# Optimization experiments

Measured on AMD Instinct MI355X. Metric: run time of the kernel, lower is better.

## Reference

```python
import jax, jax.numpy as jnp
import numpy as np

V, S, D, H, L, F = 32000, 1024, 1024, 16, 6, 4096
DH = D // H          # 64
HALF = DH // 2       # 32
EPS = 1e-5
ROPE_BASE = 10000.0


def setup_inputs() -> dict:
    key = jax.random.key(0)
    ks = jax.random.split(key, 16)
    std = 0.02
    inp = {
        "tokens": jax.random.randint(ks[0], (4, S), 0, V),
        "tok_emb": jax.random.normal(ks[1], (V, D), jnp.float32) * std,
        "ln1_s": jnp.ones((L, D), jnp.float32),
        "ln1_b": jnp.zeros((L, D), jnp.float32),
        "w_qkv": jax.random.normal(ks[2], (L, D, 3 * D), jnp.float32) * std,
        "w_proj": jax.random.normal(ks[3], (L, D, D), jnp.float32) * std,
        "ln2_s": jnp.ones((L, D), jnp.float32),
        "ln2_b": jnp.zeros((L, D), jnp.float32),
        "w_in": jax.random.normal(ks[4], (L, D, 2 * F), jnp.float32) * std,
        "w_out": jax.random.normal(ks[5], (L, F, D), jnp.float32) * std,
        "lnf_s": jnp.ones((D,), jnp.float32),
        "lnf_b": jnp.zeros((D,), jnp.float32),
        "w_score": jax.random.normal(ks[6], (D, 1), jnp.float32) * std,
        "w_cls": jax.random.normal(ks[7], (D, S), jnp.float32) * std,
    }
    return inp


def _layernorm(x, s, b):
    m = x.mean(-1, keepdims=True)
    v = ((x - m) ** 2).mean(-1, keepdims=True)
    return (x - m) * jax.lax.rsqrt(v + EPS) * s + b


def _rotate_half(x):
    x_even = x[..., ::2]
    x_odd = x[..., 1::2]
    return jnp.stack((-x_odd, x_even), axis=-1).reshape(x.shape)


def _rope_tables():
    inv_freq = 1.0 / (ROPE_BASE ** (jnp.arange(0, DH, 2, dtype=jnp.float32) / DH))
    pos = jnp.arange(S, dtype=jnp.float32)
    freqs = jnp.outer(pos, inv_freq)               # [S, DH/2]
    cos = jnp.repeat(jnp.cos(freqs), 2, axis=-1)   # [S, DH]
    sin = jnp.repeat(jnp.sin(freqs), 2, axis=-1)
    return cos, sin


def _forward(tokens, tok_emb, ln1_s, ln1_b, w_qkv, w_proj, ln2_s, ln2_b,
             w_in, w_out, lnf_s, lnf_b, w_score, w_cls):
    B = tokens.shape[0]
    cos, sin = _rope_tables()                      # [S, DH], broadcast over B,H
    lower = jnp.tril(jnp.ones((S, S), jnp.bool_))  # j <= i -> "down" subspace
    scale = HALF ** -0.5

    h = tok_emb[tokens]                            # [B, S, D]

    def block(h, p):
        l1s, l1b, Wqkv, Wp, l2s, l2b, Wi, Wo = p
        # --- dual-triangle attention ---
        qkv = _layernorm(h, l1s, l1b) @ Wqkv       # [B, S, 3D]
        q, k, v = jnp.split(qkv, 3, axis=-1)
        def heads(t):
            return t.reshape(B, S, H, DH).transpose(0, 2, 1, 3)  # [B,H,S,DH]
        q, k, v = heads(q), heads(k), heads(v)
        q = q * cos + _rotate_half(q) * sin
        k = k * cos + _rotate_half(k) * sin
        a_up = jnp.einsum('bhqd,bhkd->bhqk', q[..., :HALF], k[..., :HALF]) * scale
        a_dn = jnp.einsum('bhqd,bhkd->bhqk', q[..., HALF:], k[..., HALF:]) * scale
        logits = jnp.where(lower, a_dn, a_up)
        w = jax.nn.softmax(logits, axis=-1)
        o = jnp.einsum('bhqk,bhkd->bhqd', w, v)
        o = o.transpose(0, 2, 1, 3).reshape(B, S, D) @ Wp
        h = h + o
        # --- SwiGLU MLP ---
        g = _layernorm(h, l2s, l2b) @ Wi           # [B, S, 2F]
        a, b = jnp.split(g, 2, axis=-1)
        h = h + (jax.nn.silu(a) * b) @ Wo
        return h, None

    h, _ = jax.lax.scan(block, h, (ln1_s, ln1_b, w_qkv, w_proj, ln2_s, ln2_b, w_in, w_out))

    # pooling head: per-position scores -> softmax over positions -> weighted sum
    h = _layernorm(h, lnf_s, lnf_b)
    scores = h @ w_score                           # [B, S, 1]
    pw = jax.nn.softmax(scores, axis=1)
    pooled = jnp.sum(pw * h, axis=1)               # [B, D]
    return pooled @ w_cls                          # [B, S] logits over positions


def reference(tokens, tok_emb, ln1_s, ln1_b, w_qkv, w_proj, ln2_s, ln2_b,
              w_in, w_out, lnf_s, lnf_b, w_score, w_cls):
    return _forward(tokens, tok_emb, ln1_s, ln1_b, w_qkv, w_proj, ln2_s, ln2_b,
                    w_in, w_out, lnf_s, lnf_b, w_score, w_cls)
```

## Files before the change

kernel.cpp:

```cpp
#include <hip/hip_runtime.h>

#define Bsz 4
#define Ssz 1024
#define Dsz 1024
#define Hn  16
#define DHn 64
#define Ln  6
#define Fsz 4096
#define SCALE_ 0.1767766952966369f
#define LOG2E_ 1.4426950408889634f

typedef unsigned long long u64;
typedef __attribute__((ext_vector_type(8))) short bf16x8;
typedef __attribute__((ext_vector_type(4))) float f32x4;

__device__ __forceinline__ unsigned short f2bf(float f) {
  union { float f; unsigned int u; } v; v.f = f;
  unsigned int u = v.u + 0x7fffu + ((v.u >> 16) & 1u);
  return (unsigned short)(u >> 16);
}
__device__ __forceinline__ float bf2f(unsigned short h) {
  union { unsigned int u; float f; } v; v.u = ((unsigned int)h) << 16;
  return v.f;
}
__device__ __forceinline__ void gload_lds16(const void* g, void* lds) {
  __builtin_amdgcn_global_load_lds(
      (const __attribute__((address_space(1))) unsigned int*)g,
      (__attribute__((address_space(3))) unsigned int*)lds, 16, 0, 0);
}

__device__ __forceinline__ int swz_addr(int r, int lq) {
  int line = r >> 1;
  int u = ((r & 1) << 2) | lq;
  int s = u ^ (line & 7);
  return line * 128 + s * 16;
}

__global__ __launch_bounds__(256) void k_cossin(float* __restrict__ cosT, float* __restrict__ sinT) {
  int idx = blockIdx.x * 256 + threadIdx.x;
  if (idx >= Ssz * 32) return;
  int s = idx >> 5, i = idx & 31;
  float inv = powf(10000.f, -((float)(2 * i)) / 64.f);
  float f = (float)s * inv;
  cosT[idx] = cosf(f);
  sinT[idx] = sinf(f);
}

__global__ __launch_bounds__(256) void k_embed(const int* __restrict__ tokens,
                                               const float* __restrict__ emb,
                                               float* __restrict__ h) {
  int rs = blockIdx.x;
  int t = threadIdx.x;
  int tok = tokens[rs];
  *(float4*)&h[(u64)rs * Dsz + t * 4] = *(const float4*)&emb[(u64)tok * Dsz + t * 4];
}

template <int BF16OUT>
__global__ __launch_bounds__(256) void k_layernorm(const float* __restrict__ x,
                                                   const float* __restrict__ sc,
                                                   const float* __restrict__ bi,
                                                   void* outv) {
  int row = blockIdx.x, t = threadIdx.x;
  const float* xr = x + (u64)row * Dsz;
  float4 v = *(const float4*)&xr[t * 4];
  float sm = v.x + v.y + v.z + v.w;
  float sq = v.x * v.x + v.y * v.y + v.z * v.z + v.w * v.w;
#pragma unroll
  for (int m = 1; m < 64; m <<= 1) { sm += __shfl_xor(sm, m); sq += __shfl_xor(sq, m); }
  __shared__ float r1[4], r2[4];
  if ((t & 63) == 0) { r1[t >> 6] = sm; r2[t >> 6] = sq; }
  __syncthreads();
  sm = r1[0] + r1[1] + r1[2] + r1[3];
  sq = r2[0] + r2[1] + r2[2] + r2[3];
  float mean = sm * (1.f / Dsz);
  float inv = rsqrtf(sq * (1.f / Dsz) - mean * mean + 1e-5f);
  float4 s4 = *(const float4*)&sc[t * 4];
  float4 b4 = *(const float4*)&bi[t * 4];
  float y0 = (v.x - mean) * inv * s4.x + b4.x;
  float y1 = (v.y - mean) * inv * s4.y + b4.y;
  float y2 = (v.z - mean) * inv * s4.z + b4.z;
  float y3 = (v.w - mean) * inv * s4.w + b4.w;
  if (BF16OUT) {
    ushort4 o; o.x = f2bf(y0); o.y = f2bf(y1); o.z = f2bf(y2); o.w = f2bf(y3);
    *(ushort4*)((unsigned short*)outv + (u64)row * Dsz + t * 4) = o;
  } else {
    float4 o; o.x = y0; o.y = y1; o.z = y2; o.w = y3;
    *(float4*)((float*)outv + (u64)row * Dsz + t * 4) = o;
  }
}

__global__ __launch_bounds__(256) void k_redres_ln(const float* __restrict__ p0,
                                                   const float* __restrict__ p1,
                                                   float* __restrict__ h,
                                                   const float* __restrict__ sc,
                                                   const float* __restrict__ bi,
                                                   unsigned short* __restrict__ xo) {
  int row = blockIdx.x, t = threadIdx.x;
  u64 base = (u64)row * Dsz + t * 4;
  float4 a = *(float4*)&h[base];
  float4 b0 = *(const float4*)&p0[base];
  float4 c0 = *(const float4*)&p1[base];
  a.x += b0.x + c0.x; a.y += b0.y + c0.y; a.z += b0.z + c0.z; a.w += b0.w + c0.w;
  *(float4*)&h[base] = a;
  float sm = a.x + a.y + a.z + a.w;
  float sq = a.x * a.x + a.y * a.y + a.z * a.z + a.w * a.w;
#pragma unroll
  for (int m = 1; m < 64; m <<= 1) { sm += __shfl_xor(sm, m); sq += __shfl_xor(sq, m); }
  __shared__ float r1[4], r2[4];
  if ((t & 63) == 0) { r1[t >> 6] = sm; r2[t >> 6] = sq; }
  __syncthreads();
  sm = r1[0] + r1[1] + r1[2] + r1[3];
  sq = r2[0] + r2[1] + r2[2] + r2[3];
  float mean = sm * (1.f / Dsz);
  float inv = rsqrtf(sq * (1.f / Dsz) - mean * mean + 1e-5f);
  float4 s4 = *(const float4*)&sc[t * 4];
  float4 b4 = *(const float4*)&bi[t * 4];
  ushort4 o;
  o.x = f2bf((a.x - mean) * inv * s4.x + b4.x);
  o.y = f2bf((a.y - mean) * inv * s4.y + b4.y);
  o.z = f2bf((a.z - mean) * inv * s4.z + b4.z);
  o.w = f2bf((a.w - mean) * inv * s4.w + b4.w);
  *(ushort4*)&xo[base] = o;
}

__global__ __launch_bounds__(256) void k_redres(const float* __restrict__ p0,
                                                const float* __restrict__ p1,
                                                float* __restrict__ h) {
  u64 i = ((u64)blockIdx.x * 256 + threadIdx.x) * 4;
  float4 a = *(float4*)&h[i];
  float4 b = *(const float4*)&p0[i];
  float4 c = *(const float4*)&p1[i];
  a.x += b.x + c.x; a.y += b.y + c.y; a.z += b.z + c.z; a.w += b.w + c.w;
  *(float4*)&h[i] = a;
}

__global__ __launch_bounds__(256) void k_wt(const float* __restrict__ in,
                                            unsigned short* __restrict__ out, int K, int N) {
  in += (u64)blockIdx.z * K * N;
  out += (u64)blockIdx.z * K * N;
  __shared__ float tile[32][33];
  int nb = blockIdx.x * 32, kb = blockIdx.y * 32;
  int t = threadIdx.x;
  int r = t >> 3, c4 = (t & 7) * 4;
  float4 v = *(const float4*)&in[(u64)(kb + r) * N + nb + c4];
  tile[r][c4] = v.x; tile[r][c4 + 1] = v.y; tile[r][c4 + 2] = v.z; tile[r][c4 + 3] = v.w;
  __syncthreads();
  ushort4 o;
  o.x = f2bf(tile[c4][r]); o.y = f2bf(tile[c4 + 1][r]);
  o.z = f2bf(tile[c4 + 2][r]); o.w = f2bf(tile[c4 + 3][r]);
  *(ushort4*)&out[(u64)(nb + r) * K + kb + c4] = o;
}

__global__ __launch_bounds__(256) void k_wt_pair(const float* __restrict__ in,
                                                 unsigned short* __restrict__ out) {
  in += (u64)blockIdx.z * Dsz * 2 * Fsz;
  out += (u64)blockIdx.z * 2 * Fsz * Dsz;
  __shared__ float tile[32][33];
  int nb = blockIdx.x * 32, kb = blockIdx.y * 32;
  int t = threadIdx.x;
  int r = t >> 3, c4 = (t & 7) * 4;
  int s0 = nb >> 1;
  int srccol = (c4 < 16) ? (s0 + c4) : (Fsz + s0 + (c4 - 16));
  float4 v = *(const float4*)&in[(u64)(kb + r) * (2 * Fsz) + srccol];
  tile[r][c4] = v.x; tile[r][c4 + 1] = v.y; tile[r][c4 + 2] = v.z; tile[r][c4 + 3] = v.w;
  __syncthreads();
  int sc = (r >> 1) + (r & 1) * 16;
  ushort4 o;
  o.x = f2bf(tile[c4][sc]); o.y = f2bf(tile[c4 + 1][sc]);
  o.z = f2bf(tile[c4 + 2][sc]); o.w = f2bf(tile[c4 + 3][sc]);
  *(ushort4*)&out[(u64)(nb + r) * Dsz + kb + c4] = o;
}

template <int EPI>
__global__ __launch_bounds__(256, 3)
void k_ring(const unsigned short* __restrict__ A,
            const unsigned short* __restrict__ Bt,
            const float* resid, void* Cout,
            int M, int N, int K, int KH,
            unsigned short* qr, unsigned short* kr, unsigned short* vt,
            const float* cosT, const float* sinT) {
  __shared__ char lds[3][16384] __attribute__((aligned(16)));
  int t = threadIdx.x, w = t >> 6, l = t & 63;
  int wm = w >> 1, wn = w & 1;
  int lr = l & 15, lq = l >> 4;
  int bn = blockIdx.x, bm = blockIdx.y, kz = blockIdx.z;
  int NT = KH >> 5;
  int g0 = t, g1 = t + 256;
  int L0 = g0 >> 3, u0 = (g0 & 7) ^ (L0 & 7), row0 = 2 * L0 + (u0 >> 2), kc0 = (u0 & 3) * 8;
  int L1 = g1 >> 3, u1 = (g1 & 7) ^ (L1 & 7), row1 = 2 * L1 + (u1 >> 2), kc1 = (u1 & 3) * 8;
  const unsigned short* Az = A + (u64)kz * KH;
  const unsigned short* Bz = Bt + (u64)kz * KH;
  const char* Asrc0 = (const char*)(Az + (u64)(bm * 128 + row0) * K + kc0);
  const char* Asrc1 = (const char*)(Az + (u64)(bm * 128 + row1) * K + kc1);
  const char* Bsrc0 = (const char*)(Bz + (u64)(bn * 128 + row0) * K + kc0);
  const char* Bsrc1 = (const char*)(Bz + (u64)(bn * 128 + row1) * K + kc1);
  f32x4 acc[4][4];
#pragma unroll
  for (int i = 0; i < 4; ++i)
#pragma unroll
    for (int j = 0; j < 4; ++j) acc[i][j] = (f32x4){0.f, 0.f, 0.f, 0.f};
#define STG(slot, jj) { char* d_ = lds[slot]; \
    gload_lds16(Asrc0 + (u64)(jj) * 64, d_ + g0 * 16); \
    gload_lds16(Asrc1 + (u64)(jj) * 64, d_ + g1 * 16); \
    gload_lds16(Bsrc0 + (u64)(jj) * 64, d_ + 8192 + g0 * 16); \
    gload_lds16(Bsrc1 + (u64)(jj) * 64, d_ + 8192 + g1 * 16); }
  STG(0, 0); STG(1, 1);
  int cs = 0, ss = 2;
  for (int j = 0; j < NT; ++j) {
    if (j < NT - 1) asm volatile("s_waitcnt vmcnt(4)" ::: "memory");
    else            asm volatile("s_waitcnt vmcnt(0)" ::: "memory");
    __builtin_amdgcn_s_barrier();
    __builtin_amdgcn_sched_barrier(0);
    const char* Ab = lds[cs];
    const char* Bb = lds[cs] + 8192;
    if (j + 2 < NT) STG(ss, j + 2);
    bf16x8 afrag[4], bfrag[4];
#pragma unroll
    for (int ni = 0; ni < 4; ++ni)
      bfrag[ni] = *(const bf16x8*)(Bb + swz_addr(wn * 64 + ni * 16 + lr, lq));
#pragma unroll
    for (int mi = 0; mi < 4; ++mi)
      afrag[mi] = *(const bf16x8*)(Ab + swz_addr(wm * 64 + mi * 16 + lr, lq));
    __builtin_amdgcn_s_setprio(1);
#pragma unroll
    for (int mi = 0; mi < 4; ++mi)
#pragma unroll
      for (int ni = 0; ni < 4; ++ni)
        acc[mi][ni] = __builtin_amdgcn_mfma_f32_16x16x32_bf16(afrag[mi], bfrag[ni], acc[mi][ni], 0, 0, 0);
    __builtin_amdgcn_s_setprio(0);
    cs = (cs == 2) ? 0 : cs + 1;
    ss = (ss == 2) ? 0 : ss + 1;
  }
#undef STG
  u64 zoff = (u64)kz * M * N;
#pragma unroll
  for (int mi = 0; mi < 4; ++mi)
#pragma unroll
    for (int ni = 0; ni < 4; ++ni)
#pragma unroll
      for (int r = 0; r < 4; ++r) {
        int row = bm * 128 + wm * 64 + mi * 16 + lq * 4 + r;
        int col = bn * 128 + wn * 64 + ni * 16 + lr;
        float v = acc[mi][ni][r];
        if (EPI == 3) {
          float pv = __shfl_xor(v, 1);
          if ((lr & 1) == 0) {
            float res = v / (1.f + __expf(-v)) * pv;
            ((unsigned short*)Cout)[(u64)row * (N >> 1) + (col >> 1)] = f2bf(res);
          }
        } else if (EPI == 4) {
          float pv = __shfl_xor(v, 1);
          int b = row >> 10, s = row & 1023;
          int sec = col >> 10, c = col & 1023, hh = c >> 6, dh = c & 63;
          if (sec == 2) {
            vt[((u64)(b * Hn + hh) * DHn + dh) * Ssz + s] = f2bf(v);
          } else {
            int ci = s * 32 + (dh >> 1);
            float cs_ = cosT[ci], sn_ = sinT[ci];
            float out = (dh & 1) ? (v * cs_ + pv * sn_) : (v * cs_ - pv * sn_);
            u64 dst = ((u64)(b * Hn + hh) * Ssz + s) * DHn + dh;
            (sec == 0 ? qr : kr)[dst] = f2bf(out);
          }
        } else {
          u64 idx = (u64)row * N + col;
          if (EPI == 0) ((float*)Cout)[zoff + idx] = v;
          else if (EPI == 1) ((unsigned short*)Cout)[idx] = f2bf(v);
          else ((float*)Cout)[idx] = resid[idx] + v;
        }
      }
}

__global__ __launch_bounds__(256) void k_attn(const unsigned short* __restrict__ qr,
                                              const unsigned short* __restrict__ kr,
                                              const unsigned short* __restrict__ vt,
                                              unsigned short* __restrict__ outp) {
  __shared__ unsigned short Klds[2][2][64 * 32] __attribute__((aligned(16)));
  __shared__ unsigned short Vlds[2][2][64 * 32] __attribute__((aligned(16)));
  __shared__ unsigned short Plds[4][16 * 64] __attribute__((aligned(16)));
  int qt = blockIdx.x, hh = blockIdx.y, b = blockIdx.z;
  int t = threadIdx.x, w = t >> 6, l = t & 63;
  int lr = l & 15, lq = l >> 4;
  u64 bh = (u64)(b * Hn + hh);
  const unsigned short* Qp = qr + bh * (Ssz * DHn);
  const unsigned short* Kp = kr + bh * (Ssz * DHn);
  const unsigned short* Vp = vt + bh * ((u64)DHn * Ssz);
  int q0 = qt * 64 + w * 16;
  bf16x8 qlo = *(const bf16x8*)&Qp[(q0 + lr) * DHn + lq * 8];
  bf16x8 qhi = *(const bf16x8*)&Qp[(q0 + lr) * DHn + 32 + lq * 8];
  int srow = t >> 2;
  int scol8 = (t & 3) * 8;
#define STAGEKV(bufi, kbase)                                                         \
  do {                                                                               \
    gload_lds16(&Kp[((kbase) + srow) * 64 + scol8],      (char*)&Klds[bufi][0][0] + t * 16); \
    gload_lds16(&Kp[((kbase) + srow) * 64 + 32 + scol8], (char*)&Klds[bufi][1][0] + t * 16); \
    gload_lds16(&Vp[(u64)srow * Ssz + (kbase) + scol8],      (char*)&Vlds[bufi][0][0] + t * 16); \
    gload_lds16(&Vp[(u64)srow * Ssz + (kbase) + 32 + scol8], (char*)&Vlds[bufi][1][0] + t * 16); \
  } while (0)
  float m_col = -1e30f, lsum = 0.f;
  float m_row[4] = {-1e30f, -1e30f, -1e30f, -1e30f};
  f32x4 o[4];
#pragma unroll
  for (int r = 0; r < 4; ++r) o[r] = (f32x4){0.f, 0.f, 0.f, 0.f};
  char* Pw = (char*)&Plds[w][0];

  STAGEKV(0, 0);
  asm volatile("s_waitcnt vmcnt(0)" ::: "memory");
  __syncthreads();
  int buf = 0;
  const float lsc = SCALE_ * LOG2E_;
  for (int kb = 0; kb < Ssz; kb += 64) {
    if (kb + 64 < Ssz) STAGEKV(buf ^ 1, kb + 64);
    float p[4][4];
#pragma unroll
    for (int ct = 0; ct < 4; ++ct) {
      int kc = kb + ct * 16;
      f32x4 z = (f32x4){0.f, 0.f, 0.f, 0.f};
      if (kc < q0) {
        bf16x8 khi = *(const bf16x8*)&Klds[buf][1][(ct * 16 + lr) * 32 + lq * 8];
        f32x4 shi = __builtin_amdgcn_mfma_f32_16x16x32_bf16(khi, qhi, z, 0, 0, 0);
#pragma unroll
        for (int r = 0; r < 4; ++r) p[ct][r] = shi[r] * lsc;
      } else if (kc > q0) {
        bf16x8 klo = *(const bf16x8*)&Klds[buf][0][(ct * 16 + lr) * 32 + lq * 8];
        f32x4 slo = __builtin_amdgcn_mfma_f32_16x16x32_bf16(klo, qlo, z, 0, 0, 0);
#pragma unroll
        for (int r = 0; r < 4; ++r) p[ct][r] = slo[r] * lsc;
      } else {
        bf16x8 klo = *(const bf16x8*)&Klds[buf][0][(ct * 16 + lr) * 32 + lq * 8];
        bf16x8 khi = *(const bf16x8*)&Klds[buf][1][(ct * 16 + lr) * 32 + lq * 8];
        f32x4 slo = __builtin_amdgcn_mfma_f32_16x16x32_bf16(klo, qlo, z, 0, 0, 0);
        f32x4 shi = __builtin_amdgcn_mfma_f32_16x16x32_bf16(khi, qhi, z, 0, 0, 0);
        int kg0 = kc + lq * 4;
        int qg = q0 + lr;
#pragma unroll
        for (int r = 0; r < 4; ++r) p[ct][r] = (kg0 + r <= qg ? shi[r] : slo[r]) * lsc;
      }
    }
    float tm = p[0][0];
#pragma unroll
    for (int ct = 0; ct < 4; ++ct)
#pragma unroll
      for (int r = 0; r < 4; ++r) tm = fmaxf(tm, p[ct][r]);
    tm = fmaxf(tm, __shfl_xor(tm, 16));
    tm = fmaxf(tm, __shfl_xor(tm, 32));
    if (__any(tm > m_col)) {
      float m_new = fmaxf(m_col, tm);
      lsum *= exp2f(m_col - m_new);
      m_col = m_new;
#pragma unroll
      for (int r = 0; r < 4; ++r) {
        float mr = __shfl(m_col, lq * 4 + r);
        float scf = exp2f(m_row[r] - mr);
        m_row[r] = mr;
        o[0][r] *= scf; o[1][r] *= scf; o[2][r] *= scf; o[3][r] *= scf;
      }
    }
#pragma unroll
    for (int ct = 0; ct < 4; ++ct) {
      float e0 = exp2f(p[ct][0] - m_col);
      float e1 = exp2f(p[ct][1] - m_col);
      float e2 = exp2f(p[ct][2] - m_col);
      float e3 = exp2f(p[ct][3] - m_col);
      lsum += e0 + e1 + e2 + e3;
      ushort4 pk; pk.x = f2bf(e0); pk.y = f2bf(e1); pk.z = f2bf(e2); pk.w = f2bf(e3);
      int byte_ = (lr * 128 + ct * 32 + lq * 8) ^ ((lr & 7) << 4);
      *(ushort4*)(Pw + byte_) = pk;
    }
    asm volatile("s_waitcnt lgkmcnt(0)" ::: "memory");
    __builtin_amdgcn_sched_barrier(0);
#pragma unroll
    for (int ks = 0; ks < 2; ++ks) {
      int pb = (lr * 128 + ks * 64 + lq * 16) ^ ((lr & 7) << 4);
      bf16x8 pa = *(const bf16x8*)(Pw + pb);
#pragma unroll
      for (int nt = 0; nt < 4; ++nt) {
        bf16x8 vb = *(const bf16x8*)&Vlds[buf][ks][(nt * 16 + lr) * 32 + lq * 8];
        o[nt] = __builtin_amdgcn_mfma_f32_16x16x32_bf16(pa, vb, o[nt], 0, 0, 0);
      }
    }
    asm volatile("s_waitcnt vmcnt(0)" ::: "memory");
    __syncthreads();
    buf ^= 1;
  }
  lsum += __shfl_xor(lsum, 16);
  lsum += __shfl_xor(lsum, 32);
  u64 obase = ((u64)b * Ssz) * Dsz + (u64)hh * DHn;
#pragma unroll
  for (int r = 0; r < 4; ++r) {
    float ls = __shfl(lsum, lq * 4 + r);
    float inv = 1.f / ls;
    int qrow = q0 + lq * 4 + r;
#pragma unroll
    for (int nt = 0; nt < 4; ++nt)
      outp[obase + (u64)qrow * Dsz + nt * 16 + lr] = f2bf(o[nt][r] * inv);
  }
#undef STAGEKV
}

__global__ __launch_bounds__(256) void k_scores(const float* __restrict__ hf,
                                                const float* __restrict__ wsc,
                                                float* __restrict__ scores) {
  int row = blockIdx.x * 4 + (threadIdx.x >> 6);
  int l = threadIdx.x & 63;
  const float* xr = hf + (u64)row * Dsz;
  float acc = 0.f;
#pragma unroll
  for (int j = 0; j < 4; ++j) {
    float4 v = *(const float4*)&xr[(j * 64 + l) * 4];
    float4 ww = *(const float4*)&wsc[(j * 64 + l) * 4];
    acc += v.x * ww.x + v.y * ww.y + v.z * ww.z + v.w * ww.w;
  }
#pragma unroll
  for (int m = 1; m < 64; m <<= 1) acc += __shfl_xor(acc, m);
  if (l == 0) scores[row] = acc;
}

__global__ __launch_bounds__(256) void k_softmax_s(const float* __restrict__ sc,
                                                   float* __restrict__ pw) {
  int b = blockIdx.x, t = threadIdx.x;
  const float* sr = sc + b * Ssz;
  float4 v = *(const float4*)&sr[t * 4];
  float mx = fmaxf(fmaxf(v.x, v.y), fmaxf(v.z, v.w));
#pragma unroll
  for (int m = 1; m < 64; m <<= 1) mx = fmaxf(mx, __shfl_xor(mx, m));
  __shared__ float red[4];
  if ((t & 63) == 0) red[t >> 6] = mx;
  __syncthreads();
  mx = fmaxf(fmaxf(red[0], red[1]), fmaxf(red[2], red[3]));
  float e0 = __expf(v.x - mx), e1 = __expf(v.y - mx), e2 = __expf(v.z - mx), e3 = __expf(v.w - mx);
  float sm = e0 + e1 + e2 + e3;
#pragma unroll
  for (int m = 1; m < 64; m <<= 1) sm += __shfl_xor(sm, m);
  __shared__ float red2[4];
  if ((t & 63) == 0) red2[t >> 6] = sm;
  __syncthreads();
  sm = red2[0] + red2[1] + red2[2] + red2[3];
  float inv = 1.f / sm;
  float4 o; o.x = e0 * inv; o.y = e1 * inv; o.z = e2 * inv; o.w = e3 * inv;
  *(float4*)&pw[b * Ssz + t * 4] = o;
}

__global__ __launch_bounds__(256) void k_pool1(const float* __restrict__ hf,
                                               const float* __restrict__ pw,
                                               float* __restrict__ part) {
  int d = blockIdx.x * 256 + threadIdx.x;
  int b = blockIdx.y, scn = blockIdx.z;
  const float* pwb = pw + b * Ssz + scn * 64;
  const float* hb = hf + ((u64)(b * Ssz + scn * 64)) * Dsz + d;
  float acc = 0.f;
#pragma unroll 4
  for (int s = 0; s < 64; ++s) acc += pwb[s] * hb[(u64)s * Dsz];
  part[(u64)(b * 16 + scn) * Dsz + d] = acc;
}
__global__ __launch_bounds__(256) void k_pool2(const float* __restrict__ part,
                                               float* __restrict__ pooled) {
  int d = blockIdx.x * 256 + threadIdx.x;
  int b = blockIdx.y;
  float acc = 0.f;
#pragma unroll
  for (int i = 0; i < 16; ++i) acc += part[(u64)(b * 16 + i) * Dsz + d];
  pooled[b * Dsz + d] = acc;
}

__global__ __launch_bounds__(256) void k_cls1(const float* __restrict__ pooled,
                                              const float* __restrict__ wcls,
                                              float* __restrict__ part) {
  int n = blockIdx.x * 64 + (threadIdx.x & 63);
  int b = threadIdx.x >> 6;
  int kz = blockIdx.y;
  const float* pb = pooled + b * Dsz + kz * 128;
  const float* wb = wcls + (u64)(kz * 128) * Ssz + n;
  float acc = 0.f;
#pragma unroll 4
  for (int k = 0; k < 128; ++k) acc += pb[k] * wb[(u64)k * Ssz];
  part[(u64)(kz * 4 + b) * Ssz + n] = acc;
}
__global__ __launch_bounds__(256) void k_cls2(const float* __restrict__ part,
                                              float* __restrict__ outp) {
  int n = blockIdx.x * 64 + (threadIdx.x & 63);
  int b = threadIdx.x >> 6;
  float acc = 0.f;
#pragma unroll
  for (int kz = 0; kz < 8; ++kz) acc += part[(u64)(kz * 4 + b) * Ssz + n];
  outp[b * Ssz + n] = acc;
}

extern "C" void kernel_launch(void* const* d_in, const int* in_sizes, int n_in,
                              void* d_out, int out_size, void* d_ws, size_t ws_size,
                              hipStream_t stream) {
  (void)in_sizes; (void)n_in; (void)out_size; (void)ws_size;
  const int*   tokens  = (const int*)  d_in[0];
  const float* tok_emb = (const float*)d_in[1];
  const float* ln1_s   = (const float*)d_in[2];
  const float* ln1_b   = (const float*)d_in[3];
  const float* w_qkv   = (const float*)d_in[4];
  const float* w_proj  = (const float*)d_in[5];
  const float* ln2_s   = (const float*)d_in[6];
  const float* ln2_b   = (const float*)d_in[7];
  const float* w_in    = (const float*)d_in[8];
  const float* w_out   = (const float*)d_in[9];
  const float* lnf_s   = (const float*)d_in[10];
  const float* lnf_b   = (const float*)d_in[11];
  const float* w_score = (const float*)d_in[12];
  const float* w_cls   = (const float*)d_in[13];
  float* outp = (float*)d_out;
  char* ws = (char*)d_ws;

  unsigned short* q_r    = (unsigned short*)(ws + 25165824ull);
  unsigned short* k_r    = (unsigned short*)(ws + 33554432ull);
  unsigned short* v_t    = (unsigned short*)(ws + 41943040ull);
  unsigned short* a_out  = (unsigned short*)(ws + 50331648ull);
  float*          hf     = (float*)(ws + 0);
  unsigned short* x_ln   = (unsigned short*)(ws + 67108864ull);
  unsigned short* mbuf   = (unsigned short*)(ws + 75497472ull);
  float*          h      = (float*)(ws + 109051904ull);
  float* cosT    = (float*)(ws + 125829120ull);
  float* sinT    = (float*)(ws + 125960192ull);
  float* scoresb = (float*)(ws + 126091264ull);
  float* pwb     = (float*)(ws + 126107648ull);
  float* pooledb = (float*)(ws + 126124032ull);
  float* poolpart= (float*)(ws + 126140416ull);
  float* clspart = (float*)(ws + 126402560ull);
  unsigned short* wqkv_t = (unsigned short*)(ws + 134217728ull);
  unsigned short* wproj_t= (unsigned short*)(ws + 171966464ull);
  unsigned short* win_t  = (unsigned short*)(ws + 184549376ull);
  unsigned short* wout_t = (unsigned short*)(ws + 285212672ull);
  float* skpart  = (float*)(ws + 335544320ull);

  dim3 blk(256);
  k_cossin<<<dim3(128), blk, 0, stream>>>(cosT, sinT);
  k_embed<<<dim3(4096), blk, 0, stream>>>(tokens, tok_emb, h);
  k_wt<<<dim3(96, 32, 6), blk, 0, stream>>>(w_qkv, wqkv_t, Dsz, 3 * Dsz);
  k_wt<<<dim3(32, 32, 6), blk, 0, stream>>>(w_proj, wproj_t, Dsz, Dsz);
  k_wt_pair<<<dim3(256, 32, 6), blk, 0, stream>>>(w_in, win_t);
  k_wt<<<dim3(32, 128, 6), blk, 0, stream>>>(w_out, wout_t, Fsz, Dsz);

  k_layernorm<1><<<dim3(4096), blk, 0, stream>>>(h, ln1_s, ln1_b, (void*)x_ln);
  for (int l = 0; l < Ln; ++l) {
    unsigned short* wq = wqkv_t + (u64)l * 3145728ull;
    unsigned short* wp = wproj_t + (u64)l * 1048576ull;
    unsigned short* wi = win_t + (u64)l * 8388608ull;
    unsigned short* wo = wout_t + (u64)l * 4194304ull;
    k_ring<4><<<dim3(24, 32), blk, 0, stream>>>(x_ln, wq, nullptr, nullptr,
        4096, 3072, 1024, 1024, q_r, k_r, v_t, cosT, sinT);
    k_attn<<<dim3(16, 16, 4), blk, 0, stream>>>(q_r, k_r, v_t, a_out);
    k_ring<2><<<dim3(8, 32), blk, 0, stream>>>(a_out, wp, h, (void*)h,
        4096, 1024, 1024, 1024, nullptr, nullptr, nullptr, nullptr, nullptr);
    k_layernorm<1><<<dim3(4096), blk, 0, stream>>>(h, ln2_s + l * Dsz, ln2_b + l * Dsz, (void*)x_ln);
    k_ring<3><<<dim3(64, 32), blk, 0, stream>>>(x_ln, wi, nullptr, (void*)mbuf,
        4096, 8192, 1024, 1024, nullptr, nullptr, nullptr, nullptr, nullptr);
    k_ring<0><<<dim3(8, 32, 2), blk, 0, stream>>>(mbuf, wo, nullptr, (void*)skpart,
        4096, 1024, 4096, 2048, nullptr, nullptr, nullptr, nullptr, nullptr);
    if (l < Ln - 1)
      k_redres_ln<<<dim3(4096), blk, 0, stream>>>(skpart, skpart + 4194304ull, h,
          ln1_s + (l + 1) * Dsz, ln1_b + (l + 1) * Dsz, x_ln);
    else
      k_redres<<<dim3(4096), blk, 0, stream>>>(skpart, skpart + 4194304ull, h);
  }

  k_layernorm<0><<<dim3(4096), blk, 0, stream>>>(h, lnf_s, lnf_b, (void*)hf);
  k_scores<<<dim3(1024), blk, 0, stream>>>(hf, w_score, scoresb);
  k_softmax_s<<<dim3(4), blk, 0, stream>>>(scoresb, pwb);
  k_pool1<<<dim3(4, 4, 16), blk, 0, stream>>>(hf, pwb, poolpart);
  k_pool2<<<dim3(4, 4), blk, 0, stream>>>(poolpart, pooledb);
  k_cls1<<<dim3(16, 8), blk, 0, stream>>>(pooledb, w_cls, clspart);
  k_cls2<<<dim3(16), blk, 0, stream>>>(clspart, outp);
}
```

Measured before the change: 1.963 ms.

## Add 256x256-tile pipelined GEMM kernel for MLP up/down projections

Introduces a new 512-thread GEMM kernel with 256x256 output tiles, double-buffered LDS staging via direct global-to-LDS loads, and explicit vmcnt waits interleaved with MFMA phases. The SwiGLU up-projection and the down-projection now use it, and the down-projection split-K goes from 2 to 4 partitions, so the residual-reduce kernels sum four partials. Larger tiles are meant to raise data reuse and MFMA density in the dominant MLP GEMMs. In exchange they use heavy register and LDS budgets and launch fewer blocks, and the extra split-K partials add memory traffic in the reduction.

```diff
diff --git a/kernel.cpp b/kernel.cpp
--- a/kernel.cpp
+++ b/kernel.cpp
@@ -34,6 +34,10 @@
   int u = ((r & 1) << 2) | lq;
   int s = u ^ (line & 7);
   return line * 128 + s * 16;
+}
+
+__device__ __forceinline__ bf16x8 frag_read(const char* base, int row, int lq) {
+  return *(const bf16x8*)(base + row * 64 + ((lq ^ (row & 3)) * 16));
 }
 
 __global__ __launch_bounds__(256) void k_cossin(float* __restrict__ cosT, float* __restrict__ sinT) {
@@ -89,8 +93,8 @@
   }
 }
 
-__global__ __launch_bounds__(256) void k_redres_ln(const float* __restrict__ p0,
-                                                   const float* __restrict__ p1,
+#define PARTN 4194304ull
+__global__ __launch_bounds__(256) void k_redres_ln(const float* __restrict__ p,
                                                    float* __restrict__ h,
                                                    const float* __restrict__ sc,
                                                    const float* __restrict__ bi,
@@ -98,9 +102,11 @@
   int row = blockIdx.x, t = threadIdx.x;
   u64 base = (u64)row * Dsz + t * 4;
   float4 a = *(float4*)&h[base];
-  float4 b0 = *(const float4*)&p0[base];
-  float4 c0 = *(const float4*)&p1[base];
-  a.x += b0.x + c0.x; a.y += b0.y + c0.y; a.z += b0.z + c0.z; a.w += b0.w + c0.w;
+#pragma unroll
+  for (int z = 0; z < 4; ++z) {
+    float4 q = *(const float4*)&p[z * PARTN + base];
+    a.x += q.x; a.y += q.y; a.z += q.z; a.w += q.w;
+  }
   *(float4*)&h[base] = a;
   float sm = a.x + a.y + a.z + a.w;
   float sq = a.x * a.x + a.y * a.y + a.z * a.z + a.w * a.w;
@@ -123,14 +129,15 @@
   *(ushort4*)&xo[base] = o;
 }
 
-__global__ __launch_bounds__(256) void k_redres(const float* __restrict__ p0,
-                                                const float* __restrict__ p1,
+__global__ __launch_bounds__(256) void k_redres(const float* __restrict__ p,
                                                 float* __restrict__ h) {
   u64 i = ((u64)blockIdx.x * 256 + threadIdx.x) * 4;
   float4 a = *(float4*)&h[i];
-  float4 b = *(const float4*)&p0[i];
-  float4 c = *(const float4*)&p1[i];
-  a.x += b.x + c.x; a.y += b.y + c.y; a.z += b.z + c.z; a.w += b.w + c.w;
+#pragma unroll
+  for (int z = 0; z < 4; ++z) {
+    float4 q = *(const float4*)&p[z * PARTN + i];
+    a.x += q.x; a.y += q.y; a.z += q.z; a.w += q.w;
+  }
   *(float4*)&h[i] = a;
 }
 
@@ -232,7 +239,6 @@
     ss = (ss == 2) ? 0 : ss + 1;
   }
 #undef STG
-  u64 zoff = (u64)kz * M * N;
 #pragma unroll
   for (int mi = 0; mi < 4; ++mi)
 #pragma unroll
@@ -242,13 +248,7 @@
         int row = bm * 128 + wm * 64 + mi * 16 + lq * 4 + r;
         int col = bn * 128 + wn * 64 + ni * 16 + lr;
         float v = acc[mi][ni][r];
-        if (EPI == 3) {
-          float pv = __shfl_xor(v, 1);
-          if ((lr & 1) == 0) {
-            float res = v / (1.f + __expf(-v)) * pv;
-            ((unsigned short*)Cout)[(u64)row * (N >> 1) + (col >> 1)] = f2bf(res);
-          }
-        } else if (EPI == 4) {
+        if (EPI == 4) {
           float pv = __shfl_xor(v, 1);
           int b = row >> 10, s = row & 1023;
           int sec = col >> 10, c = col & 1023, hh = c >> 6, dh = c & 63;
@@ -263,9 +263,124 @@
           }
         } else {
           u64 idx = (u64)row * N + col;
-          if (EPI == 0) ((float*)Cout)[zoff + idx] = v;
-          else if (EPI == 1) ((unsigned short*)Cout)[idx] = f2bf(v);
+          if (EPI == 1) ((unsigned short*)Cout)[idx] = f2bf(v);
           else ((float*)Cout)[idx] = resid[idx] + v;
+        }
+      }
+}
+
+#define VM8 asm volatile("s_waitcnt vmcnt(8)" ::: "memory")
+#define VM4 asm volatile("s_waitcnt vmcnt(4)" ::: "memory")
+#define VM0 asm volatile("s_waitcnt vmcnt(0)" ::: "memory")
+#define VMN
+
+#define STGP(buf_, kh_, j_) { \
+    char* dA = lds[buf_] + (kh_) * 16384; \
+    char* dB = lds[buf_] + 32768 + (kh_) * 16384; \
+    u64 ko = (u64)((j_) * 64 + (kh_) * 32) * 2; \
+    gload_lds16(Ab0 + ko, dA + t * 16); \
+    gload_lds16(Ab1 + ko, dA + 8192 + t * 16); \
+    gload_lds16(Bb0 + ko, dB + t * 16); \
+    gload_lds16(Bb1 + ko, dB + 8192 + t * 16); }
+
+#define MFMA16(mibase) \
+  _Pragma("unroll") for (int mi = 0; mi < 4; ++mi) \
+    _Pragma("unroll") for (int ni = 0; ni < 4; ++ni) \
+      acc[mi + (mibase)][ni] = __builtin_amdgcn_mfma_f32_16x16x32_bf16(afr[mi], bfr[ni], acc[mi + (mibase)][ni], 0, 0, 0);
+
+#define PH_COMPUTE(mibase) \
+  __builtin_amdgcn_s_barrier(); \
+  asm volatile("s_waitcnt lgkmcnt(0)" ::: "memory"); \
+  __builtin_amdgcn_sched_barrier(0); \
+  __builtin_amdgcn_s_setprio(1); \
+  MFMA16(mibase); \
+  __builtin_amdgcn_s_setprio(0);
+
+#define TILE256(jj, S1, S3, G1, G3) { \
+  const int buf_ = (jj) & 1, kf_ = (jj) & 1, ks2_ = kf_ ^ 1; \
+  const char* LA_ = lds[buf_]; \
+  const char* LB_ = lds[buf_] + 32768; \
+  bf16x8 afr[4], bfr[4]; \
+   \
+  _Pragma("unroll") for (int ni = 0; ni < 4; ++ni) \
+    bfr[ni] = frag_read(LB_ + kf_ * 16384, wn * 64 + ni * 16 + lr, lq); \
+  _Pragma("unroll") for (int mi = 0; mi < 4; ++mi) \
+    afr[mi] = frag_read(LA_ + kf_ * 16384, wm * 128 + mi * 16 + lr, lq); \
+  PH_COMPUTE(0); \
+  __builtin_amdgcn_s_barrier(); \
+   \
+  _Pragma("unroll") for (int mi = 0; mi < 4; ++mi) \
+    afr[mi] = frag_read(LA_ + kf_ * 16384, wm * 128 + (mi + 4) * 16 + lr, lq); \
+  if (S1) STGP(buf_ ^ 1, kf_, (jj) + 1); \
+  PH_COMPUTE(4); \
+  G1; \
+  __builtin_amdgcn_s_barrier(); \
+   \
+  _Pragma("unroll") for (int ni = 0; ni < 4; ++ni) \
+    bfr[ni] = frag_read(LB_ + ks2_ * 16384, wn * 64 + ni * 16 + lr, lq); \
+  _Pragma("unroll") for (int mi = 0; mi < 4; ++mi) \
+    afr[mi] = frag_read(LA_ + ks2_ * 16384, wm * 128 + mi * 16 + lr, lq); \
+  PH_COMPUTE(0); \
+  __builtin_amdgcn_s_barrier(); \
+   \
+  _Pragma("unroll") for (int mi = 0; mi < 4; ++mi) \
+    afr[mi] = frag_read(LA_ + ks2_ * 16384, wm * 128 + (mi + 4) * 16 + lr, lq); \
+  if (S3) STGP(buf_, kf_, (jj) + 2); \
+  PH_COMPUTE(4); \
+  G3; \
+  __builtin_amdgcn_s_barrier(); \
+}
+
+template <int EPI>
+__global__ __launch_bounds__(512, 2)
+void k_g256(const unsigned short* __restrict__ A,
+            const unsigned short* __restrict__ Bt,
+            void* Cout, int M, int N, int K, int KH) {
+  __shared__ char lds[2][65536] __attribute__((aligned(16)));
+  int t = threadIdx.x, w = t >> 6, l = t & 63;
+  int wm = w >> 2, wn = w & 3;
+  int lr = l & 15, lq = l >> 4;
+  int bn = blockIdx.x, bm = blockIdx.y, kz = blockIdx.z;
+  int NT = KH >> 6;
+  int r0 = t >> 2, sl = t & 3;
+  int c0 = (sl ^ (r0 & 3)) * 8;
+  const unsigned short* Az = A + (u64)kz * KH;
+  const unsigned short* Bz = Bt + (u64)kz * KH;
+  const char* Ab0 = (const char*)(Az + (u64)(bm * 256 + r0) * K + c0);
+  const char* Ab1 = (const char*)(Az + (u64)(bm * 256 + 128 + r0) * K + c0);
+  const char* Bb0 = (const char*)(Bz + (u64)(bn * 256 + r0) * K + c0);
+  const char* Bb1 = (const char*)(Bz + (u64)(bn * 256 + 128 + r0) * K + c0);
+  f32x4 acc[8][4];
+#pragma unroll
+  for (int i = 0; i < 8; ++i)
+#pragma unroll
+    for (int j = 0; j < 4; ++j) acc[i][j] = (f32x4){0.f, 0.f, 0.f, 0.f};
+  STGP(0, 0, 0);
+  STGP(0, 1, 0);
+  STGP(1, 1, 1);
+  VM8;
+  __builtin_amdgcn_s_barrier();
+  for (int j = 0; j < NT - 2; ++j) TILE256(j, 1, 1, VM8, VM8);
+  TILE256(NT - 2, 1, 0, VM8, VM4);
+  TILE256(NT - 1, 0, 0, VM0, VMN);
+  u64 zoff = (u64)kz * M * N;
+#pragma unroll
+  for (int mi = 0; mi < 8; ++mi)
+#pragma unroll
+    for (int ni = 0; ni < 4; ++ni)
+#pragma unroll
+      for (int r = 0; r < 4; ++r) {
+        int row = bm * 256 + wm * 128 + mi * 16 + lq * 4 + r;
+        int col = bn * 256 + wn * 64 + ni * 16 + lr;
+        float v = acc[mi][ni][r];
+        if (EPI == 3) {
+          float pv = __shfl_xor(v, 1);
+          if ((lr & 1) == 0) {
+            float res = v / (1.f + __expf(-v)) * pv;
+            ((unsigned short*)Cout)[(u64)row * (N >> 1) + (col >> 1)] = f2bf(res);
+          }
+        } else {
+          ((float*)Cout)[zoff + (u64)row * N + col] = v;
         }
       }
 }
@@ -547,15 +662,13 @@
     k_ring<2><<<dim3(8, 32), blk, 0, stream>>>(a_out, wp, h, (void*)h,
         4096, 1024, 1024, 1024, nullptr, nullptr, nullptr, nullptr, nullptr);
     k_layernorm<1><<<dim3(4096), blk, 0, stream>>>(h, ln2_s + l * Dsz, ln2_b + l * Dsz, (void*)x_ln);
-    k_ring<3><<<dim3(64, 32), blk, 0, stream>>>(x_ln, wi, nullptr, (void*)mbuf,
-        4096, 8192, 1024, 1024, nullptr, nullptr, nullptr, nullptr, nullptr);
-    k_ring<0><<<dim3(8, 32, 2), blk, 0, stream>>>(mbuf, wo, nullptr, (void*)skpart,
-        4096, 1024, 4096, 2048, nullptr, nullptr, nullptr, nullptr, nullptr);
+    k_g256<3><<<dim3(32, 16), dim3(512), 0, stream>>>(x_ln, wi, (void*)mbuf, 4096, 8192, 1024, 1024);
+    k_g256<0><<<dim3(4, 16, 4), dim3(512), 0, stream>>>(mbuf, wo, (void*)skpart, 4096, 1024, 4096, 1024);
     if (l < Ln - 1)
-      k_redres_ln<<<dim3(4096), blk, 0, stream>>>(skpart, skpart + 4194304ull, h,
+      k_redres_ln<<<dim3(4096), blk, 0, stream>>>(skpart, h,
           ln1_s + (l + 1) * Dsz, ln1_b + (l + 1) * Dsz, x_ln);
     else
-      k_redres<<<dim3(4096), blk, 0, stream>>>(skpart, skpart + 4194304ull, h);
+      k_redres<<<dim3(4096), blk, 0, stream>>>(skpart, h);
   }
 
   k_layernorm<0><<<dim3(4096), blk, 0, stream>>>(h, lnf_s, lnf_b, (void*)hf);
```

Result: no change. 1.943 ms (-1.0%).
